# Optimization experiments

Measured on AMD Instinct MI355X. Metric: run time of the kernel, lower is better.

Reference implementation:

```python
import jax, jax.numpy as jnp
import numpy as np

N_ATOMS, N_EDGES, N_TRIPLES = 5000, 200000, 4000000
D_NODE, D_EDGE, N_BASIS = 128, 128, 9


def setup_inputs() -> dict:
    key = jax.random.key(0)
    ks = jax.random.split(key, 14)
    inp = {
        "node_feat": jax.random.normal(ks[0], (N_ATOMS, D_NODE), jnp.float32),
        "edge_feat": jax.random.normal(ks[1], (N_EDGES, D_EDGE), jnp.float32),
        "three_basis": jax.random.normal(ks[2], (N_TRIPLES, N_BASIS), jnp.float32),
        "three_cutoff": jax.random.uniform(ks[3], (N_EDGES,), jnp.float32),
        # learned params: update_network_atom = Linear(d_node->n_basis) + sigmoid
        "W_atom": jax.random.normal(ks[4], (D_NODE, N_BASIS), jnp.float32) / np.sqrt(D_NODE).astype(np.float32),
        "b_atom": jnp.zeros((N_BASIS,), jnp.float32),
        # update_network_bond = gated MLP: silu(Linear) * sigmoid(Linear), n_basis->d_edge
        "W_gate": jax.random.normal(ks[5], (N_BASIS, D_EDGE), jnp.float32) / np.sqrt(N_BASIS).astype(np.float32),
        "b_gate": jnp.zeros((D_EDGE,), jnp.float32),
        "W_sig": jax.random.normal(ks[6], (N_BASIS, D_EDGE), jnp.float32) / np.sqrt(N_BASIS).astype(np.float32),
        "b_sig": jnp.zeros((D_EDGE,), jnp.float32),
        # graph structure (int constants)
        "graph_dst": jax.random.randint(ks[7], (N_EDGES,), 0, N_ATOMS, jnp.int32),
        "lg_src": jax.random.randint(ks[8], (N_TRIPLES,), 0, N_EDGES, jnp.int32),
        "lg_dst": jax.random.randint(ks[9], (N_TRIPLES,), 0, N_EDGES, jnp.int32),
        # sorted segment ids == get_segment_indices_from_n(n_triple_ij)
        "segment_ids": jnp.sort(jax.random.randint(ks[10], (N_TRIPLES,), 0, N_EDGES, jnp.int32)),
    }
    return inp


def reference(node_feat, edge_feat, three_basis, three_cutoff,
              W_atom, b_atom, W_gate, b_gate, W_sig, b_sig,
              graph_dst, lg_src, lg_dst, segment_ids):
    # Eq.2: transform node features, gather end atom of each triple's second bond
    atoms = jax.nn.sigmoid(node_feat @ W_atom + b_atom)          # [n_atoms, n_basis]
    end_atom_index = graph_dst[lg_dst]                           # [n_triples]
    basis = three_basis * atoms[end_atom_index]                  # [n_triples, n_basis]
    # cutoff weights per triple (dead code in the provided source: scatter uses basis)
    weights = three_cutoff[lg_src] * three_cutoff[lg_dst]        # [n_triples]
    _ = basis * weights[:, None]
    # scatter-sum triples back to their bond
    new_bonds = jax.ops.segment_sum(basis, segment_ids, num_segments=N_EDGES)  # [n_edges, n_basis]
    # Eq.3: gated MLP bond update
    update = jax.nn.silu(new_bonds @ W_gate + b_gate) * jax.nn.sigmoid(new_bonds @ W_sig + b_sig)
    return edge_feat + update
```

## Files before the change

kernel.cpp:

```cpp
#include <hip/hip_runtime.h>

#define D_NODE  128
#define N_BASIS 9
#define D_EDGE  128

__device__ __forceinline__ float fast_sigmoid(float x) {
    return __builtin_amdgcn_rcpf(1.0f + __expf(-x));
}

__global__ __launch_bounds__(256) void atoms_kernel(
    const float* __restrict__ node_feat,
    const float* __restrict__ W_atom,
    const float* __restrict__ b_atom,
    float* __restrict__ atoms, int n_atoms)
{
    __shared__ float sW[D_NODE * N_BASIS];
    for (int t = threadIdx.x; t < D_NODE * N_BASIS; t += 256)
        sW[t] = W_atom[t];
    __syncthreads();
    int idx = blockIdx.x * 256 + threadIdx.x;
    int total = n_atoms * N_BASIS;
    if (idx >= total) return;
    int a = idx / N_BASIS;
    int b = idx - a * N_BASIS;
    const float* row = node_feat + a * D_NODE;
    float acc = b_atom[b];
#pragma unroll 8
    for (int i = 0; i < D_NODE; ++i)
        acc += row[i] * sW[i * N_BASIS + b];
    atoms[idx] = fast_sigmoid(acc);
}

__global__ __launch_bounds__(256) void rowptr_kernel(
    const int* __restrict__ seg, int* __restrict__ row_ptr,
    int n_triples, int n_edges)
{
    int i = blockIdx.x * 256 + threadIdx.x;
    if (i >= n_triples) return;
    int cur  = seg[i];
    int prev = (i == 0) ? -1 : seg[i - 1];
    for (int s = prev + 1; s <= cur; ++s) row_ptr[s] = i;
    if (i == n_triples - 1) {
        for (int s = cur + 1; s <= n_edges; ++s) row_ptr[s] = n_triples;
    }
}

__global__ __launch_bounds__(256) void edge_kernel(
    const float* __restrict__ edge_feat,
    const float* __restrict__ three_basis,
    const float* __restrict__ atoms,
    const int*   __restrict__ graph_dst,
    const int*   __restrict__ lg_dst,
    const int*   __restrict__ row_ptr,
    const float* __restrict__ W_gate, const float* __restrict__ b_gate,
    const float* __restrict__ W_sig,  const float* __restrict__ b_sig,
    float* __restrict__ out, int n_edges)
{
    int wave = threadIdx.x >> 6;
    int lane = threadIdx.x & 63;
    int e = blockIdx.x * 4 + wave;
    if (e >= n_edges) return;

    int start = row_ptr[e];
    int end   = row_ptr[e + 1];

    float acc[N_BASIS];
#pragma unroll
    for (int k = 0; k < N_BASIS; ++k) acc[k] = 0.0f;

    for (int t = start + lane; t < end; t += 64) {
        int atom = graph_dst[lg_dst[t]];
        const float* tb = three_basis + (size_t)t * N_BASIS;
        const float* at = atoms + atom * N_BASIS;
#pragma unroll
        for (int k = 0; k < N_BASIS; ++k)
            acc[k] += tb[k] * at[k];
    }

#pragma unroll
    for (int off = 1; off < 64; off <<= 1) {
#pragma unroll
        for (int k = 0; k < N_BASIS; ++k)
            acc[k] += __shfl_xor(acc[k], off, 64);
    }

    const float* efr  = edge_feat + (size_t)e * D_EDGE;
    float*       outr = out       + (size_t)e * D_EDGE;
#pragma unroll
    for (int h = 0; h < 2; ++h) {
        int j = lane + h * 64;
        float g = b_gate[j];
        float s = b_sig[j];
#pragma unroll
        for (int k = 0; k < N_BASIS; ++k) {
            g += acc[k] * W_gate[k * D_EDGE + j];
            s += acc[k] * W_sig[k * D_EDGE + j];
        }
        float silu = g * fast_sigmoid(g);
        outr[j] = efr[j] + silu * fast_sigmoid(s);
    }
}

extern "C" void kernel_launch(void* const* d_in, const int* in_sizes, int n_in,
                              void* d_out, int out_size, void* d_ws, size_t ws_size,
                              hipStream_t stream) {
    const float* node_feat   = (const float*)d_in[0];
    const float* edge_feat   = (const float*)d_in[1];
    const float* three_basis = (const float*)d_in[2];
    const float* W_atom      = (const float*)d_in[4];
    const float* b_atom      = (const float*)d_in[5];
    const float* W_gate      = (const float*)d_in[6];
    const float* b_gate      = (const float*)d_in[7];
    const float* W_sig       = (const float*)d_in[8];
    const float* b_sig       = (const float*)d_in[9];
    const int*   graph_dst   = (const int*)d_in[10];
    const int*   lg_dst      = (const int*)d_in[12];
    const int*   seg         = (const int*)d_in[13];

    int n_atoms   = in_sizes[0] / D_NODE;
    int n_edges   = in_sizes[1] / D_EDGE;
    int n_triples = in_sizes[2] / N_BASIS;

    float* atoms = (float*)d_ws;
    size_t atoms_bytes = ((size_t)n_atoms * N_BASIS * sizeof(float) + 255) & ~(size_t)255;
    int* row_ptr = (int*)((char*)d_ws + atoms_bytes);

    float* out = (float*)d_out;

    atoms_kernel<<<(n_atoms * N_BASIS + 255) / 256, 256, 0, stream>>>(
        node_feat, W_atom, b_atom, atoms, n_atoms);

    rowptr_kernel<<<(n_triples + 255) / 256, 256, 0, stream>>>(
        seg, row_ptr, n_triples, n_edges);

    edge_kernel<<<(n_edges + 3) / 4, 256, 0, stream>>>(
        edge_feat, three_basis, atoms, graph_dst, lg_dst, row_ptr,
        W_gate, b_gate, W_sig, b_sig, out, n_edges);
}
```

Measured before the change: 469.4 us.

## Replace per-edge wave reduction with triple-parallel segmented LDS scatter and separate MLP

Drops the row_ptr build and the one-wave-per-edge reduction. A triple-parallel kernel now has each thread load four triples with vectorized loads, run a segmented sum, and accumulate into LDS per block, then flush to global with atomics only at block-boundary segments. A separate vectorized MLP kernel reads the reduced new_bonds. This targets the low lane utilization of the per-edge kernel, which averages about 20 triples per 64-lane wave, and its shuffle reductions. The cost is an extra global round trip for new_bonds, a memset, and atomics, plus float summation order that is no longer deterministic.

```diff
diff --git a/kernel.cpp b/kernel.cpp
--- a/kernel.cpp
+++ b/kernel.cpp
@@ -3,6 +3,11 @@
 #define D_NODE  128
 #define N_BASIS 9
 #define D_EDGE  128
+
+#define BLOCK_C 256
+#define TPT     4
+#define CHUNK   (BLOCK_C * TPT)
+#define SEG_CAP 512
 
 __device__ __forceinline__ float fast_sigmoid(float x) {
     return __builtin_amdgcn_rcpf(1.0f + __expf(-x));
@@ -31,74 +36,155 @@
     atoms[idx] = fast_sigmoid(acc);
 }
 
-__global__ __launch_bounds__(256) void rowptr_kernel(
-    const int* __restrict__ seg, int* __restrict__ row_ptr,
-    int n_triples, int n_edges)
-{
-    int i = blockIdx.x * 256 + threadIdx.x;
-    if (i >= n_triples) return;
-    int cur  = seg[i];
-    int prev = (i == 0) ? -1 : seg[i - 1];
-    for (int s = prev + 1; s <= cur; ++s) row_ptr[s] = i;
-    if (i == n_triples - 1) {
-        for (int s = cur + 1; s <= n_edges; ++s) row_ptr[s] = n_triples;
-    }
-}
-
-__global__ __launch_bounds__(256) void edge_kernel(
-    const float* __restrict__ edge_feat,
+__global__ __launch_bounds__(BLOCK_C) void triple_kernel(
     const float* __restrict__ three_basis,
     const float* __restrict__ atoms,
     const int*   __restrict__ graph_dst,
     const int*   __restrict__ lg_dst,
-    const int*   __restrict__ row_ptr,
+    const int*   __restrict__ seg,
+    float* __restrict__ new_bonds,
+    int n_triples)
+{
+    __shared__ float lacc[SEG_CAP * N_BASIS];
+    __shared__ int sh_first, sh_last;
+
+    const int tid = threadIdx.x;
+    const int chunk_start = blockIdx.x * CHUNK;
+    const int t0 = chunk_start + tid * TPT;
+
+    if (tid == 0) sh_first = seg[chunk_start];
+    if (tid == BLOCK_C - 1) {
+        int last = chunk_start + CHUNK;
+        if (last > n_triples) last = n_triples;
+        sh_last = seg[last - 1];
+    }
+    for (int i = tid; i < SEG_CAP * N_BASIS; i += BLOCK_C)
+        lacc[i] = 0.0f;
+    __syncthreads();
+
+    const int seg_first = sh_first;
+    const int range = sh_last - seg_first + 1;
+    const bool use_lds = (range <= SEG_CAP);
+
+    if (t0 < n_triples) {
+        const int nt = min(TPT, n_triples - t0);
+
+        float tbv[TPT * N_BASIS];
+        int sgs[TPT];
+        int lds_idx[TPT];
+
+        if (nt == TPT) {
+            const float4* tb4 = (const float4*)(three_basis + (size_t)t0 * N_BASIS);
+#pragma unroll
+            for (int q = 0; q < 9; ++q)
+                *(float4*)&tbv[q * 4] = tb4[q];
+            int4 sg = *(const int4*)(seg + t0);
+            sgs[0] = sg.x; sgs[1] = sg.y; sgs[2] = sg.z; sgs[3] = sg.w;
+            int4 ld = *(const int4*)(lg_dst + t0);
+            lds_idx[0] = ld.x; lds_idx[1] = ld.y; lds_idx[2] = ld.z; lds_idx[3] = ld.w;
+        } else {
+            for (int i = 0; i < nt; ++i) {
+                sgs[i] = seg[t0 + i];
+                lds_idx[i] = lg_dst[t0 + i];
+                for (int k = 0; k < N_BASIS; ++k)
+                    tbv[i * N_BASIS + k] = three_basis[(size_t)(t0 + i) * N_BASIS + k];
+            }
+        }
+
+        float sum[N_BASIS];
+        int cur = sgs[0];
+#pragma unroll
+        for (int k = 0; k < N_BASIS; ++k) sum[k] = 0.0f;
+
+#pragma unroll
+        for (int i = 0; i < TPT; ++i) {
+            if (i >= nt) break;
+            if (sgs[i] != cur) {
+                if (use_lds) {
+                    float* dst = lacc + (cur - seg_first) * N_BASIS;
+#pragma unroll
+                    for (int k = 0; k < N_BASIS; ++k) unsafeAtomicAdd(&dst[k], sum[k]);
+                } else {
+                    float* dst = new_bonds + (size_t)cur * N_BASIS;
+#pragma unroll
+                    for (int k = 0; k < N_BASIS; ++k) unsafeAtomicAdd(&dst[k], sum[k]);
+                }
+                cur = sgs[i];
+#pragma unroll
+                for (int k = 0; k < N_BASIS; ++k) sum[k] = 0.0f;
+            }
+            int atom = graph_dst[lds_idx[i]];
+            const float* arow = atoms + atom * N_BASIS;
+#pragma unroll
+            for (int k = 0; k < N_BASIS; ++k)
+                sum[k] += tbv[i * N_BASIS + k] * arow[k];
+        }
+        if (use_lds) {
+            float* dst = lacc + (cur - seg_first) * N_BASIS;
+#pragma unroll
+            for (int k = 0; k < N_BASIS; ++k) unsafeAtomicAdd(&dst[k], sum[k]);
+        } else {
+            float* dst = new_bonds + (size_t)cur * N_BASIS;
+#pragma unroll
+            for (int k = 0; k < N_BASIS; ++k) unsafeAtomicAdd(&dst[k], sum[k]);
+        }
+    }
+
+    __syncthreads();
+
+    if (use_lds) {
+        int total = range * N_BASIS;
+        for (int idx = tid; idx < total; idx += BLOCK_C) {
+            int r = idx / N_BASIS;
+            int k = idx - r * N_BASIS;
+            float v = lacc[idx];
+            int s = seg_first + r;
+            if (r == 0 || r == range - 1) {
+                if (v != 0.0f)
+                    unsafeAtomicAdd(&new_bonds[(size_t)s * N_BASIS + k], v);
+            } else {
+                new_bonds[(size_t)s * N_BASIS + k] = v;
+            }
+        }
+    }
+}
+
+__global__ __launch_bounds__(256) void mlp_kernel(
+    const float* __restrict__ edge_feat,
+    const float* __restrict__ new_bonds,
     const float* __restrict__ W_gate, const float* __restrict__ b_gate,
     const float* __restrict__ W_sig,  const float* __restrict__ b_sig,
     float* __restrict__ out, int n_edges)
 {
-    int wave = threadIdx.x >> 6;
-    int lane = threadIdx.x & 63;
-    int e = blockIdx.x * 4 + wave;
+    const int tid = threadIdx.x;
+    const int grp = tid >> 5;
+    const int c   = (tid & 31) * 4;
+    const int e   = blockIdx.x * 8 + grp;
     if (e >= n_edges) return;
 
-    int start = row_ptr[e];
-    int end   = row_ptr[e + 1];
-
-    float acc[N_BASIS];
-#pragma unroll
-    for (int k = 0; k < N_BASIS; ++k) acc[k] = 0.0f;
-
-    for (int t = start + lane; t < end; t += 64) {
-        int atom = graph_dst[lg_dst[t]];
-        const float* tb = three_basis + (size_t)t * N_BASIS;
-        const float* at = atoms + atom * N_BASIS;
-#pragma unroll
-        for (int k = 0; k < N_BASIS; ++k)
-            acc[k] += tb[k] * at[k];
-    }
-
-#pragma unroll
-    for (int off = 1; off < 64; off <<= 1) {
-#pragma unroll
-        for (int k = 0; k < N_BASIS; ++k)
-            acc[k] += __shfl_xor(acc[k], off, 64);
-    }
-
-    const float* efr  = edge_feat + (size_t)e * D_EDGE;
-    float*       outr = out       + (size_t)e * D_EDGE;
-#pragma unroll
-    for (int h = 0; h < 2; ++h) {
-        int j = lane + h * 64;
-        float g = b_gate[j];
-        float s = b_sig[j];
-#pragma unroll
-        for (int k = 0; k < N_BASIS; ++k) {
-            g += acc[k] * W_gate[k * D_EDGE + j];
-            s += acc[k] * W_sig[k * D_EDGE + j];
-        }
-        float silu = g * fast_sigmoid(g);
-        outr[j] = efr[j] + silu * fast_sigmoid(s);
-    }
+    float nb[N_BASIS];
+    const float* nbr = new_bonds + (size_t)e * N_BASIS;
+#pragma unroll
+    for (int k = 0; k < N_BASIS; ++k) nb[k] = nbr[k];
+
+    float4 g = *(const float4*)(b_gate + c);
+    float4 s = *(const float4*)(b_sig + c);
+#pragma unroll
+    for (int k = 0; k < N_BASIS; ++k) {
+        float4 wg = *(const float4*)(W_gate + k * D_EDGE + c);
+        float4 ws = *(const float4*)(W_sig  + k * D_EDGE + c);
+        g.x += nb[k] * wg.x; g.y += nb[k] * wg.y;
+        g.z += nb[k] * wg.z; g.w += nb[k] * wg.w;
+        s.x += nb[k] * ws.x; s.y += nb[k] * ws.y;
+        s.z += nb[k] * ws.z; s.w += nb[k] * ws.w;
+    }
+    float4 ef = *(const float4*)(edge_feat + (size_t)e * D_EDGE + c);
+    float4 o;
+    o.x = ef.x + g.x * fast_sigmoid(g.x) * fast_sigmoid(s.x);
+    o.y = ef.y + g.y * fast_sigmoid(g.y) * fast_sigmoid(s.y);
+    o.z = ef.z + g.z * fast_sigmoid(g.z) * fast_sigmoid(s.z);
+    o.w = ef.w + g.w * fast_sigmoid(g.w) * fast_sigmoid(s.w);
+    *(float4*)(out + (size_t)e * D_EDGE + c) = o;
 }
 
 extern "C" void kernel_launch(void* const* d_in, const int* in_sizes, int n_in,
@@ -123,17 +209,17 @@
 
     float* atoms = (float*)d_ws;
     size_t atoms_bytes = ((size_t)n_atoms * N_BASIS * sizeof(float) + 255) & ~(size_t)255;
-    int* row_ptr = (int*)((char*)d_ws + atoms_bytes);
-
-    float* out = (float*)d_out;
+    float* new_bonds = (float*)((char*)d_ws + atoms_bytes);
+    size_t nb_bytes = (size_t)n_edges * N_BASIS * sizeof(float);
+
+    hipMemsetAsync(new_bonds, 0, nb_bytes, stream);
 
     atoms_kernel<<<(n_atoms * N_BASIS + 255) / 256, 256, 0, stream>>>(
         node_feat, W_atom, b_atom, atoms, n_atoms);
 
-    rowptr_kernel<<<(n_triples + 255) / 256, 256, 0, stream>>>(
-        seg, row_ptr, n_triples, n_edges);
-
-    edge_kernel<<<(n_edges + 3) / 4, 256, 0, stream>>>(
-        edge_feat, three_basis, atoms, graph_dst, lg_dst, row_ptr,
-        W_gate, b_gate, W_sig, b_sig, out, n_edges);
-}
+    triple_kernel<<<(n_triples + CHUNK - 1) / CHUNK, BLOCK_C, 0, stream>>>(
+        three_basis, atoms, graph_dst, lg_dst, seg, new_bonds, n_triples);
+
+    mlp_kernel<<<(n_edges + 7) / 8, 256, 0, stream>>>(
+        edge_feat, new_bonds, W_gate, b_gate, W_sig, b_sig, out_size ? (float*)d_out : (float*)d_out, n_edges);
+}
```

Result: slower. 519.5 us (+10.7%).
